# Kernel tuning notes

Measured on AMD Instinct MI355X. Metric: run time of the kernel, lower is better.

The kernel has to match this reference:

```python
import jax, jax.numpy as jnp
import numpy as np
import math

E = 8          # num_experts (= max_expert_num)
M = 1024       # hidden_size
H = 4096       # expert FFN dim (4*hidden)
B, S = 4, 4096 # batch, seq
CAP_FACTOR = 1.0
MIN_CAPACITY = 4


def setup_inputs() -> dict:
    key = jax.random.key(0)
    ks = jax.random.split(key, 5)
    hidden_states = jax.random.normal(ks[0], (B, S, M), dtype=jnp.float32)
    wg = jax.random.normal(ks[1], (M, E), dtype=jnp.float32) * (M ** -0.5)  # gate Linear (no bias, as in TopKGate)
    w1 = jax.random.normal(ks[2], (E, M, H), dtype=jnp.float32) * (M ** -0.5)
    b1 = jnp.zeros((E, H), dtype=jnp.float32)
    w2 = jax.random.normal(ks[3], (E, H, M), dtype=jnp.float32) * (H ** -0.5)
    b2 = jnp.zeros((E, M), dtype=jnp.float32)
    return {"hidden_states": hidden_states, "wg": wg, "w1": w1, "b1": b1, "w2": w2, "b2": b2}


def reference(hidden_states, wg, w1, b1, w2, b2):
    b, s_len, m = hidden_states.shape
    x = hidden_states.reshape(-1, m)            # [s, m], s = tokens
    s = x.shape[0]
    capacity = max(int(math.ceil(s / E * CAP_FACTOR)), MIN_CAPACITY)  # static

    # ---- top-1 gating (DeepSpeed top1gating, fp32, no jitter, no RTS) ----
    logits = x.astype(jnp.float32) @ wg          # [s, e]
    gates = jax.nn.softmax(logits, axis=1)
    idx = jnp.argmax(gates, axis=1)              # chosen expert per token
    mask1 = jax.nn.one_hot(idx, E, dtype=jnp.float32)
    exp_counts = jnp.sum(mask1, axis=0).astype(jnp.int32)
    ce = jnp.mean(mask1, axis=0)                 # fraction routed per expert (pre-drop)
    me = jnp.mean(gates, axis=0)
    l_aux = jnp.sum(me * ce) * E                 # load-balancing loss

    # position of each token within its expert's queue; drop past capacity
    locations = jnp.cumsum(mask1, axis=0) - 1.0  # [s, e]
    loc = jnp.sum(locations * mask1, axis=1).astype(jnp.int32)  # [s]
    keep = (loc < capacity).astype(jnp.float32)  # capacity drop mask
    gate_s = jnp.sum(gates * mask1, axis=1) * keep
    loc_c = jnp.clip(loc, 0, capacity - 1)

    # ---- dispatch: scatter tokens to [E, C, M] slots (equiv. to einsum('sec,sm->ecm')) ----
    dispatched = jnp.zeros((E, capacity, m), dtype=x.dtype).at[idx, loc_c].add(x * keep[:, None])

    # ---- grouped expert GEMMs (MLP with GELU) ----
    h = jax.nn.gelu(jnp.einsum('ecm,emh->ech', dispatched, w1) + b1[:, None, :])
    eout = jnp.einsum('ech,ehm->ecm', h, w2) + b2[:, None, :]

    # ---- combine: gather back and scale by gate value (dropped tokens -> 0) ----
    out = eout[idx, loc_c] * gate_s[:, None]     # [s, m]
    return out.reshape(b, s_len, m), l_aux, exp_counts
```

## Files before the change

### kernel.cpp

```cpp
#include <hip/hip_runtime.h>
#include <hip/hip_bf16.h>

#define TOKENS 16384
#define MDIM   1024
#define HDIM   4096
#define NEXP   8
#define EGRP   4
#define CAP    2048
#define NKT1   (MDIM / 64)
#define NKT2   (HDIM / 64)

typedef __attribute__((ext_vector_type(8))) short bf16x8;
typedef __attribute__((ext_vector_type(4))) float f32x4;

__device__ __forceinline__ short f2bf(float x) {
  unsigned u = __float_as_uint(x);
  unsigned r = (u + 0x7fffu + ((u >> 16) & 1u)) >> 16;
  return (short)r;
}

__device__ __forceinline__ unsigned bfbits(float x) {
  unsigned u = __float_as_uint(x);
  return u + 0x7fffu + ((u >> 16) & 1u);
}

__device__ __forceinline__ float gelu_f(float x) {
  float u = 1.5957691216057308f * (x + 0.044715f * x * x * x);
  float e = __expf(u);
  return x * (1.f - 1.f / (e + 1.f));
}

__global__ __launch_bounds__(256) void gating_kernel(
    const float* __restrict__ x, const float* __restrict__ wg,
    int* __restrict__ idx, float* __restrict__ gate,
    float* __restrict__ mepart, short* __restrict__ xb) {
  __shared__ float me_s[NEXP];
  int tid = threadIdx.x, wid = tid >> 6, lane = tid & 63;
  if (tid < NEXP) me_s[tid] = 0.f;
  __syncthreads();
  int t = blockIdx.x * 4 + wid;
  float acc[NEXP];
#pragma unroll
  for (int e = 0; e < NEXP; e++) acc[e] = 0.f;
  const float4* xr = (const float4*)(x + (size_t)t * MDIM);
  short* xbr = xb + (size_t)t * MDIM + lane * 16;
#pragma unroll
  for (int j = 0; j < 4; j++) {
    float4 xv = xr[lane * 4 + j];
    short4 bv; bv.x = f2bf(xv.x); bv.y = f2bf(xv.y); bv.z = f2bf(xv.z); bv.w = f2bf(xv.w);
    ((short4*)(xbr))[j] = bv;
    int base = lane * 16 + j * 4;
    const float* xp = &xv.x;
#pragma unroll
    for (int i = 0; i < 4; i++) {
      float xi = xp[i];
      const float4* wr = (const float4*)(wg + (size_t)(base + i) * NEXP);
      float4 w0 = wr[0], w1 = wr[1];
      acc[0] += xi * w0.x; acc[1] += xi * w0.y; acc[2] += xi * w0.z; acc[3] += xi * w0.w;
      acc[4] += xi * w1.x; acc[5] += xi * w1.y; acc[6] += xi * w1.z; acc[7] += xi * w1.w;
    }
  }
#pragma unroll
  for (int off = 32; off > 0; off >>= 1)
#pragma unroll
    for (int e = 0; e < NEXP; e++) acc[e] += __shfl_xor(acc[e], off, 64);
  if (lane == 0) {
    float mx = acc[0]; int ai = 0;
#pragma unroll
    for (int e = 1; e < NEXP; e++) if (acc[e] > mx) { mx = acc[e]; ai = e; }
    float ex[NEXP]; float se = 0.f;
#pragma unroll
    for (int e = 0; e < NEXP; e++) { ex[e] = __expf(acc[e] - mx); se += ex[e]; }
    float inv = 1.f / se;
#pragma unroll
    for (int e = 0; e < NEXP; e++) atomicAdd(&me_s[e], ex[e] * inv);
    idx[t] = ai;
    gate[t] = inv;
  }
  __syncthreads();
  if (tid < NEXP) mepart[blockIdx.x * NEXP + tid] = me_s[tid];
}

__global__ __launch_bounds__(1024) void scan_kernel(
    const int* __restrict__ idx, float* __restrict__ gate,
    int* __restrict__ s2t, int* __restrict__ counts) {
  __shared__ int wcnt[16][NEXP];
  __shared__ int wbase[16][NEXP];
  int tid = threadIdx.x, wid = tid >> 6, lane = tid & 63;
  unsigned long long ltmask = (1ull << lane) - 1ull;
  int myexp[16], myloc[16];
  int cnt[NEXP];
#pragma unroll
  for (int e = 0; e < NEXP; e++) cnt[e] = 0;
  int base_tok = wid * 1024;
#pragma unroll
  for (int p = 0; p < 16; p++) {
    int e = idx[base_tok + p * 64 + lane];
    myexp[p] = e;
    int pos = 0;
#pragma unroll
    for (int e2 = 0; e2 < NEXP; e2++) {
      unsigned long long b = __ballot(e == e2);
      if (e == e2) pos = cnt[e2] + __popcll(b & ltmask);
      cnt[e2] += __popcll(b);
    }
    myloc[p] = pos;
  }
  if (lane < NEXP) wcnt[wid][lane] = cnt[lane];
  __syncthreads();
  if (tid < 128) {
    int w = tid >> 3, e = tid & 7;
    int s = 0;
    for (int w2 = 0; w2 < w; w2++) s += wcnt[w2][e];
    wbase[w][e] = s;
  }
  __syncthreads();
#pragma unroll
  for (int p = 0; p < 16; p++) {
    int i = base_tok + p * 64 + lane;
    int e = myexp[p];
    int loc = wbase[wid][e] + myloc[p];
    if (loc < CAP) s2t[e * CAP + loc] = i;
    else           gate[i] = 0.f;
  }
  if (tid < NEXP) {
    int tot = 0;
#pragma unroll
    for (int w = 0; w < 16; w++) tot += wcnt[w][tid];
    counts[tid] = tot;
  }
}

__global__ __launch_bounds__(256) void finalize_kernel(
    const float* __restrict__ mepart, const int* __restrict__ counts,
    float* __restrict__ out_tail, int nblocks) {
  __shared__ float red[256];
  __shared__ float me[NEXP];
  int tid = threadIdx.x;
  float s = 0.f;
  int e = tid & 7;
  for (int r = tid >> 3; r < nblocks; r += 32) s += mepart[r * NEXP + e];
  red[tid] = s;
  __syncthreads();
  if (tid < NEXP) {
    float tsum = 0.f;
    for (int i = tid; i < 256; i += 8) tsum += red[i];
    me[tid] = tsum;
  }
  __syncthreads();
  if (tid == 0) {
    float la = 0.f;
    for (int k = 0; k < NEXP; k++)
      la += (me[k] / (float)TOKENS) * ((float)counts[k] / (float)TOKENS);
    out_tail[0] = la * (float)NEXP;
  }
  if (tid < NEXP) out_tail[1 + tid] = (float)counts[tid];
}

__global__ __launch_bounds__(256) void transpose_cvt_kernel(
    const float* __restrict__ in, short* __restrict__ out, int R, int Cc) {
  __shared__ short tile[64][72];
  int e = blockIdx.z;
  const float* in_e = in + (size_t)e * R * Cc;
  short* out_e = out + (size_t)e * R * Cc;
  int r0 = blockIdx.y * 64, c0 = blockIdx.x * 64;
  int tid = threadIdx.x;
#pragma unroll
  for (int i = 0; i < 4; i++) {
    int linear = tid + 256 * i;
    int r = linear >> 4;
    int f4 = linear & 15;
    float4 v = *(const float4*)(in_e + (size_t)(r0 + r) * Cc + c0 + f4 * 4);
    int c = f4 * 4;
    tile[c + 0][r] = f2bf(v.x);
    tile[c + 1][r] = f2bf(v.y);
    tile[c + 2][r] = f2bf(v.z);
    tile[c + 3][r] = f2bf(v.w);
  }
  __syncthreads();
#pragma unroll
  for (int i = 0; i < 4; i++) {
    int linear = tid + 256 * i;
    int c = linear >> 4;
    int s4 = linear & 15;
    short4 s;
    s.x = tile[c][s4 * 4 + 0]; s.y = tile[c][s4 * 4 + 1];
    s.z = tile[c][s4 * 4 + 2]; s.w = tile[c][s4 * 4 + 3];
    *(short4*)(out_e + (size_t)(c0 + c) * R + r0 + s4 * 4) = s;
  }
}

__device__ __forceinline__ void pe_vm8() {
  asm volatile("s_waitcnt vmcnt(8)" ::: "memory");
  __builtin_amdgcn_s_barrier();
  asm volatile("" ::: "memory");
}
__device__ __forceinline__ void pe_vm6() {
  asm volatile("s_waitcnt vmcnt(6)" ::: "memory");
  __builtin_amdgcn_s_barrier();
  asm volatile("" ::: "memory");
}
__device__ __forceinline__ void pe_vm0() {
  asm volatile("s_waitcnt vmcnt(0)" ::: "memory");
  __builtin_amdgcn_s_barrier();
  asm volatile("" ::: "memory");
}

#define GLL(gp, lp) __builtin_amdgcn_global_load_lds(                                   \
    (const __attribute__((address_space(1))) void*)(gp),                                \
    (__attribute__((address_space(3))) void*)(lp), 16, 0, 0)

__global__ __launch_bounds__(512, 2) void gemm1_kernel(
    const short* __restrict__ xb, const int* __restrict__ s2t,
    const short* __restrict__ W1t, const float* __restrict__ b1,
    short* __restrict__ Hh, const short* __restrict__ zrow, int eg) {
  __shared__ __align__(16) short ldsA[2][256 * 64];
  __shared__ __align__(16) short ldsB[2][256 * 64];
  int bz = blockIdx.z, bm = blockIdx.y, bn = blockIdx.x;
  int e_abs = eg + bz;
  int tid = threadIdx.x, lane = tid & 63, w = tid >> 6;
  int v = tid >> 3;
  int sl = tid & 7;

  const short* aptr[4];
#pragma unroll
  for (int q = 0; q < 4; q++) {
    int r = q * 64 + v;
    int tok = s2t[e_abs * CAP + bm * 256 + r];
    const short* basep = (tok >= 0) ? (xb + (size_t)tok * MDIM) : zrow;
    aptr[q] = basep + ((sl ^ (r & 7)) * 8);
  }
  const short* Be = W1t + ((size_t)e_abs * HDIM + (size_t)bn * 256) * MDIM;
  const short* bptr[2][2];
#pragma unroll
  for (int h = 0; h < 2; h++)
#pragma unroll
    for (int j = 0; j < 2; j++) {
      int r = j * 128 + (v >> 5) * 64 + (v & 31) + h * 32;
      bptr[h][j] = Be + (size_t)r * MDIM + ((sl ^ (r & 7)) * 8);
    }
  asm volatile("" ::: "memory");

  int ldsa_base[4], ldsb_base[2][2];
#pragma unroll
  for (int q = 0; q < 4; q++) ldsa_base[q] = (q * 64 + w * 8) * 64;
#pragma unroll
  for (int h = 0; h < 2; h++)
#pragma unroll
    for (int j = 0; j < 2; j++)
      ldsb_base[h][j] = (j * 128 + h * 32 + (w >> 2) * 64 + (w & 3) * 8) * 64;

  GLL(aptr[0] + 0,        &ldsA[0][ldsa_base[0]]);
  GLL(aptr[2] + 0,        &ldsA[0][ldsa_base[2]]);
  GLL(bptr[0][0] + 0,     &ldsB[0][ldsb_base[0][0]]);
  GLL(bptr[0][1] + 0,     &ldsB[0][ldsb_base[0][1]]);
  GLL(bptr[1][0] + 0,     &ldsB[0][ldsb_base[1][0]]);
  GLL(bptr[1][1] + 0,     &ldsB[0][ldsb_base[1][1]]);
  GLL(aptr[1] + 0,        &ldsA[0][ldsa_base[1]]);
  GLL(aptr[3] + 0,        &ldsA[0][ldsa_base[3]]);
  GLL(aptr[0] + 64,       &ldsA[1][ldsa_base[0]]);
  GLL(aptr[2] + 64,       &ldsA[1][ldsa_base[2]]);
  GLL(bptr[0][0] + 64,    &ldsB[1][ldsb_base[0][0]]);
  GLL(bptr[0][1] + 64,    &ldsB[1][ldsb_base[0][1]]);
  GLL(bptr[1][0] + 64,    &ldsB[1][ldsb_base[1][0]]);
  GLL(bptr[1][1] + 64,    &ldsB[1][ldsb_base[1][1]]);
  GLL(aptr[1] + 64,       &ldsA[1][ldsa_base[1]]);
  GLL(aptr[3] + 64,       &ldsA[1][ldsa_base[3]]);
  pe_vm8();

  int wm = w >> 2, wn = w & 3;
  int ln = lane & 15, q4 = lane >> 4;
  int offk0 = ((q4 ^ (lane & 7)) * 8);
  int offk1 = (((4 + q4) ^ (lane & 7)) * 8);
  int arowbase = wm * 128 + ln;
  int browbase = wn * 64 + ln;

  f32x4 acc[8][4];
  f32x4 zero = {0.f, 0.f, 0.f, 0.f};
#pragma unroll
  for (int a = 0; a < 8; a++)
#pragma unroll
    for (int b = 0; b < 4; b++) acc[a][b] = zero;

  for (int t = 0; t < NKT1; ++t) {
    int cur = t & 1;
    const short* La = ldsA[cur];
    const short* Lb = ldsB[cur];
    int kts = (t + 2) * 64;
    bool st = (t + 2) < NKT1;
    bool steady = t < (NKT1 - 2);
    bf16x8 af[4][2], bf0[2][2], bf1[2][2];
#pragma unroll
    for (int rt = 0; rt < 4; rt++) {
      int ro = (arowbase + rt * 16) * 64;
      af[rt][0] = *(const bf16x8*)(La + ro + offk0);
      af[rt][1] = *(const bf16x8*)(La + ro + offk1);
    }
#pragma unroll
    for (int c = 0; c < 2; c++) {
      int ro = (browbase + c * 16) * 64;
      bf0[c][0] = *(const bf16x8*)(Lb + ro + offk0);
      bf0[c][1] = *(const bf16x8*)(Lb + ro + offk1);
    }
    __builtin_amdgcn_s_setprio(1);
#pragma unroll
    for (int rt = 0; rt < 4; rt++)
#pragma unroll
      for (int c = 0; c < 2; c++) {
        acc[rt][c] = __builtin_amdgcn_mfma_f32_16x16x32_bf16(bf0[c][0], af[rt][0], acc[rt][c], 0, 0, 0);
        acc[rt][c] = __builtin_amdgcn_mfma_f32_16x16x32_bf16(bf0[c][1], af[rt][1], acc[rt][c], 0, 0, 0);
      }
    __builtin_amdgcn_s_setprio(0);
    if (steady) pe_vm8(); else pe_vm0();
#pragma unroll
    for (int c = 0; c < 2; c++) {
      int ro = (browbase + (c + 2) * 16) * 64;
      bf1[c][0] = *(const bf16x8*)(Lb + ro + offk0);
      bf1[c][1] = *(const bf16x8*)(Lb + ro + offk1);
    }
    if (st) {
      GLL(aptr[0] + kts,    &ldsA[cur][ldsa_base[0]]);
      GLL(aptr[2] + kts,    &ldsA[cur][ldsa_base[2]]);
      GLL(bptr[0][0] + kts, &ldsB[cur][ldsb_base[0][0]]);
      GLL(bptr[0][1] + kts, &ldsB[cur][ldsb_base[0][1]]);
    }
    __builtin_amdgcn_s_setprio(1);
#pragma unroll
    for (int rt = 0; rt < 4; rt++)
#pragma unroll
      for (int c = 0; c < 2; c++) {
        acc[rt][c + 2] = __builtin_amdgcn_mfma_f32_16x16x32_bf16(bf1[c][0], af[rt][0], acc[rt][c + 2], 0, 0, 0);
        acc[rt][c + 2] = __builtin_amdgcn_mfma_f32_16x16x32_bf16(bf1[c][1], af[rt][1], acc[rt][c + 2], 0, 0, 0);
      }
    __builtin_amdgcn_s_setprio(0);
    if (steady) pe_vm8(); else pe_vm0();
#pragma unroll
    for (int rt = 0; rt < 4; rt++) {
      int ro = (arowbase + 64 + rt * 16) * 64;
      af[rt][0] = *(const bf16x8*)(La + ro + offk0);
      af[rt][1] = *(const bf16x8*)(La + ro + offk1);
    }
    if (st) {
      GLL(bptr[1][0] + kts, &ldsB[cur][ldsb_base[1][0]]);
      GLL(bptr[1][1] + kts, &ldsB[cur][ldsb_base[1][1]]);
    }
    __builtin_amdgcn_s_setprio(1);
#pragma unroll
    for (int rt = 0; rt < 4; rt++)
#pragma unroll
      for (int c = 0; c < 2; c++) {
        acc[4 + rt][c] = __builtin_amdgcn_mfma_f32_16x16x32_bf16(bf0[c][0], af[rt][0], acc[4 + rt][c], 0, 0, 0);
        acc[4 + rt][c] = __builtin_amdgcn_mfma_f32_16x16x32_bf16(bf0[c][1], af[rt][1], acc[4 + rt][c], 0, 0, 0);
      }
    __builtin_amdgcn_s_setprio(0);
    if (steady) pe_vm8(); else pe_vm0();
    if (st) {
      GLL(aptr[1] + kts,    &ldsA[cur][ldsa_base[1]]);
      GLL(aptr[3] + kts,    &ldsA[cur][ldsa_base[3]]);
    }
    __builtin_amdgcn_s_setprio(1);
#pragma unroll
    for (int rt = 0; rt < 4; rt++)
#pragma unroll
      for (int c = 0; c < 2; c++) {
        acc[4 + rt][c + 2] = __builtin_amdgcn_mfma_f32_16x16x32_bf16(bf1[c][0], af[rt][0], acc[4 + rt][c + 2], 0, 0, 0);
        acc[4 + rt][c + 2] = __builtin_amdgcn_mfma_f32_16x16x32_bf16(bf1[c][1], af[rt][1], acc[4 + rt][c + 2], 0, 0, 0);
      }
    __builtin_amdgcn_s_setprio(0);
    if (steady) pe_vm8(); else pe_vm0();
  }

#pragma unroll
  for (int rt = 0; rt < 8; rt++) {
    int caprow = bm * 256 + wm * 128 + rt * 16 + ln;
    size_t rowoff = ((size_t)bz * CAP + caprow) * HDIM;
#pragma unroll
    for (int c = 0; c < 4; c++) {
      int colb = bn * 256 + wn * 64 + c * 16 + q4 * 4;
      float4 bias = *(const float4*)(b1 + (size_t)e_abs * HDIM + colb);
      unsigned u0 = bfbits(gelu_f(acc[rt][c][0] + bias.x));
      unsigned u1 = bfbits(gelu_f(acc[rt][c][1] + bias.y));
      unsigned u2 = bfbits(gelu_f(acc[rt][c][2] + bias.z));
      unsigned u3 = bfbits(gelu_f(acc[rt][c][3] + bias.w));
      uint2 pk;
      pk.x = __builtin_amdgcn_perm(u1, u0, 0x07060302u);
      pk.y = __builtin_amdgcn_perm(u3, u2, 0x07060302u);
      *(uint2*)(Hh + rowoff + colb) = pk;
    }
  }
}

__global__ __launch_bounds__(512, 2) void gemm2_kernel(
    const short* __restrict__ Hh, const short* __restrict__ W2t,
    const float* __restrict__ b2, const int* __restrict__ s2t,
    const float* __restrict__ gate, float* __restrict__ out, int eg) {
  __shared__ __align__(16) short ldsA[2][128 * 64];
  __shared__ __align__(16) short ldsB[2][256 * 64];
  int bz = blockIdx.z, bm = blockIdx.y, bn = blockIdx.x;
  int e_abs = eg + bz;
  int tid = threadIdx.x, lane = tid & 63, w = tid >> 6;
  int v = tid >> 3, sl = tid & 7;
  const short* Ae = Hh + ((size_t)bz * CAP + (size_t)bm * 128) * HDIM;
  const short* Be = W2t + ((size_t)e_abs * MDIM + (size_t)bn * 256) * HDIM;
  const short* aptr[2];
#pragma unroll
  for (int h = 0; h < 2; h++) {
    int r = (v >> 5) * 64 + (v & 31) + h * 32;
    aptr[h] = Ae + (size_t)r * HDIM + ((sl ^ (r & 7)) * 8);
  }
  const short* bptr[4];
#pragma unroll
  for (int q = 0; q < 4; q++) {
    int r = q * 64 + v;
    bptr[q] = Be + (size_t)r * HDIM + ((sl ^ (r & 7)) * 8);
  }
  int ldsa_base[2], ldsb_base[4];
#pragma unroll
  for (int h = 0; h < 2; h++) ldsa_base[h] = (h * 32 + (w >> 2) * 64 + (w & 3) * 8) * 64;
#pragma unroll
  for (int q = 0; q < 4; q++) ldsb_base[q] = (q * 64 + w * 8) * 64;

  GLL(aptr[0] + 0,  &ldsA[0][ldsa_base[0]]);
  GLL(bptr[0] + 0,  &ldsB[0][ldsb_base[0]]);
  GLL(bptr[1] + 0,  &ldsB[0][ldsb_base[1]]);
  GLL(bptr[2] + 0,  &ldsB[0][ldsb_base[2]]);
  GLL(bptr[3] + 0,  &ldsB[0][ldsb_base[3]]);
  GLL(aptr[1] + 0,  &ldsA[0][ldsa_base[1]]);
  GLL(aptr[0] + 64, &ldsA[1][ldsa_base[0]]);
  GLL(bptr[0] + 64, &ldsB[1][ldsb_base[0]]);
  GLL(bptr[1] + 64, &ldsB[1][ldsb_base[1]]);
  GLL(bptr[2] + 64, &ldsB[1][ldsb_base[2]]);
  GLL(bptr[3] + 64, &ldsB[1][ldsb_base[3]]);
  asm volatile("s_waitcnt vmcnt(5)" ::: "memory");
  __builtin_amdgcn_s_barrier();
  asm volatile("" ::: "memory");

  int wm = w >> 2, wn = w & 3;
  int ln = lane & 15, q4 = lane >> 4;
  int offk0 = ((q4 ^ (lane & 7)) * 8);
  int offk1 = (((4 + q4) ^ (lane & 7)) * 8);
  int arowbase = wm * 64 + ln;
  int browbase = wn * 64 + ln;

  f32x4 acc[4][4];
  f32x4 zero = {0.f, 0.f, 0.f, 0.f};
#pragma unroll
  for (int a = 0; a < 4; a++)
#pragma unroll
    for (int b = 0; b < 4; b++) acc[a][b] = zero;

  for (int t = 0; t < NKT2; ++t) {
    int cur = t & 1;
    const short* La = ldsA[cur];
    const short* Lb = ldsB[cur];
    bool steady = t < (NKT2 - 2);
    bf16x8 af[2][2], bf[4][2];
#pragma unroll
    for (int rt = 0; rt < 2; rt++) {
      int ro = (arowbase + rt * 16) * 64;
      af[rt][0] = *(const bf16x8*)(La + ro + offk0);
      af[rt][1] = *(const bf16x8*)(La + ro + offk1);
    }
#pragma unroll
    for (int c = 0; c < 4; c++) {
      int ro = (browbase + c * 16) * 64;
      bf[c][0] = *(const bf16x8*)(Lb + ro + offk0);
      bf[c][1] = *(const bf16x8*)(Lb + ro + offk1);
    }
    if (t + 1 < NKT2) { GLL(aptr[1] + (t + 1) * 64, &ldsA[cur ^ 1][ldsa_base[1]]); }
    __builtin_amdgcn_s_setprio(1);
#pragma unroll
    for (int rt = 0; rt < 2; rt++)
#pragma unroll
      for (int c = 0; c < 4; c++) {
        acc[rt][c] = __builtin_amdgcn_mfma_f32_16x16x32_bf16(bf[c][0], af[rt][0], acc[rt][c], 0, 0, 0);
        acc[rt][c] = __builtin_amdgcn_mfma_f32_16x16x32_bf16(bf[c][1], af[rt][1], acc[rt][c], 0, 0, 0);
      }
    __builtin_amdgcn_s_setprio(0);
    if (steady) pe_vm6(); else pe_vm0();
#pragma unroll
    for (int rt = 0; rt < 2; rt++) {
      int ro = (arowbase + 32 + rt * 16) * 64;
      af[rt][0] = *(const bf16x8*)(La + ro + offk0);
      af[rt][1] = *(const bf16x8*)(La + ro + offk1);
    }
    if (t + 2 < NKT2) {
      int kts = (t + 2) * 64;
      GLL(aptr[0] + kts, &ldsA[cur][ldsa_base[0]]);
      GLL(bptr[0] + kts, &ldsB[cur][ldsb_base[0]]);
      GLL(bptr[1] + kts, &ldsB[cur][ldsb_base[1]]);
      GLL(bptr[2] + kts, &ldsB[cur][ldsb_base[2]]);
      GLL(bptr[3] + kts, &ldsB[cur][ldsb_base[3]]);
    }
    __builtin_amdgcn_s_setprio(1);
#pragma unroll
    for (int rt = 0; rt < 2; rt++)
#pragma unroll
      for (int c = 0; c < 4; c++) {
        acc[2 + rt][c] = __builtin_amdgcn_mfma_f32_16x16x32_bf16(bf[c][0], af[rt][0], acc[2 + rt][c], 0, 0, 0);
        acc[2 + rt][c] = __builtin_amdgcn_mfma_f32_16x16x32_bf16(bf[c][1], af[rt][1], acc[2 + rt][c], 0, 0, 0);
      }
    __builtin_amdgcn_s_setprio(0);
    if (steady) pe_vm6(); else pe_vm0();
  }

#pragma unroll
  for (int rt = 0; rt < 4; rt++) {
    int caprow = bm * 128 + wm * 64 + rt * 16 + ln;
    int token = s2t[e_abs * CAP + caprow];
    if (token < 0) continue;
    float g = gate[token];
    float* orow = out + (size_t)token * MDIM;
#pragma unroll
    for (int c = 0; c < 4; c++) {
      int colb = bn * 256 + wn * 64 + c * 16 + q4 * 4;
      float4 bias = *(const float4*)(b2 + (size_t)e_abs * MDIM + colb);
      float4 vv;
      vv.x = (acc[rt][c][0] + bias.x) * g;
      vv.y = (acc[rt][c][1] + bias.y) * g;
      vv.z = (acc[rt][c][2] + bias.z) * g;
      vv.w = (acc[rt][c][3] + bias.w) * g;
      *(float4*)(orow + colb) = vv;
    }
  }
}

__global__ __launch_bounds__(256) void zerodrop_kernel(
    const float* __restrict__ gate, float* __restrict__ out) {
  int t = blockIdx.x;
  if (gate[t] != 0.f) return;
  float4 z = {0.f, 0.f, 0.f, 0.f};
  ((float4*)(out + (size_t)t * MDIM))[threadIdx.x] = z;
}

extern "C" void kernel_launch(void* const* d_in, const int* in_sizes, int n_in,
                              void* d_out, int out_size, void* d_ws, size_t ws_size,
                              hipStream_t stream) {
  const float* x  = (const float*)d_in[0];
  const float* wg = (const float*)d_in[1];
  const float* w1 = (const float*)d_in[2];
  const float* b1 = (const float*)d_in[3];
  const float* w2 = (const float*)d_in[4];
  const float* b2 = (const float*)d_in[5];
  float* out = (float*)d_out;

  char* ws = (char*)d_ws;
  size_t off = 0;
  auto alloc = [&](size_t n) { char* ptr = ws + off; off += (n + 255) & ~(size_t)255; return ptr; };
  short* W1t  = (short*)alloc((size_t)NEXP * MDIM * HDIM * 2);
  short* W2t  = (short*)alloc((size_t)NEXP * MDIM * HDIM * 2);
  short* Hh   = (short*)alloc((size_t)EGRP * CAP * HDIM * 2);
  short* xb   = (short*)alloc((size_t)TOKENS * MDIM * 2);
  short* zrow = (short*)alloc((size_t)MDIM * 2);
  int*   idx  = (int*)  alloc(TOKENS * 4);
  float* gate = (float*)alloc(TOKENS * 4);
  int*   s2t  = (int*)  alloc(NEXP * CAP * 4);
  float* mep  = (float*)alloc((TOKENS / 4) * NEXP * 4);
  int*   cnts = (int*)  alloc(NEXP * 4);
  if (ws_size < off) return;

  hipMemsetAsync(s2t, 0xFF, NEXP * CAP * 4, stream);
  hipMemsetAsync(zrow, 0, MDIM * 2, stream);

  gating_kernel<<<TOKENS / 4, 256, 0, stream>>>(x, wg, idx, gate, mep, xb);
  scan_kernel<<<1, 1024, 0, stream>>>(idx, gate, s2t, cnts);
  finalize_kernel<<<1, 256, 0, stream>>>(mep, cnts, out + (size_t)TOKENS * MDIM, TOKENS / 4);
  transpose_cvt_kernel<<<dim3(HDIM / 64, MDIM / 64, NEXP), 256, 0, stream>>>(w1, W1t, MDIM, HDIM);
  transpose_cvt_kernel<<<dim3(MDIM / 64, HDIM / 64, NEXP), 256, 0, stream>>>(w2, W2t, HDIM, MDIM);
  for (int g = 0; g < 2; g++) {
    gemm1_kernel<<<dim3(HDIM / 256, CAP / 256, EGRP), 512, 0, stream>>>(xb, s2t, W1t, b1, Hh, zrow, g * EGRP);
    gemm2_kernel<<<dim3(MDIM / 256, CAP / 128, EGRP), 512, 0, stream>>>(Hh, W2t, b2, s2t, gate, out, g * EGRP);
  }
  zerodrop_kernel<<<TOKENS, 256, 0, stream>>>(gate, out);
}
```

Measured before the change: 837.7 us.

## Restructure GEMM main loops into barrier-separated LDS-read/MFMA phases; fuse finalize into scan

Reorders the gemm1 and gemm2 inner loops so each MFMA cluster is preceded by a workgroup barrier and an explicit lgkmcnt(0) wait. Global-to-LDS prefetches are moved between the compute phases, and MFMAs are ordered k-outer. This aims at a ping-pong style schedule where LDS reads and issue of global loads don't interleave with MFMA bursts, at the cost of extra barriers per iteration. Separately, the l_aux/count finalize kernel is folded into the single-block scan kernel, removing one launch.

```diff
diff --git a/kernel.cpp b/kernel.cpp
--- a/kernel.cpp
+++ b/kernel.cpp
@@ -83,9 +83,12 @@
 
 __global__ __launch_bounds__(1024) void scan_kernel(
     const int* __restrict__ idx, float* __restrict__ gate,
-    int* __restrict__ s2t, int* __restrict__ counts) {
+    int* __restrict__ s2t, int* __restrict__ counts,
+    const float* __restrict__ mepart, float* __restrict__ out_tail) {
   __shared__ int wcnt[16][NEXP];
   __shared__ int wbase[16][NEXP];
+  __shared__ int totc[NEXP];
+  __shared__ float red2[1024];
   int tid = threadIdx.x, wid = tid >> 6, lane = tid & 63;
   unsigned long long ltmask = (1ull << lane) - 1ull;
   int myexp[16], myloc[16];
@@ -128,33 +131,25 @@
 #pragma unroll
     for (int w = 0; w < 16; w++) tot += wcnt[w][tid];
     counts[tid] = tot;
-  }
-}
-
-__global__ __launch_bounds__(256) void finalize_kernel(
-    const float* __restrict__ mepart, const int* __restrict__ counts,
-    float* __restrict__ out_tail, int nblocks) {
-  __shared__ float red[256];
-  __shared__ float me[NEXP];
-  int tid = threadIdx.x;
+    totc[tid] = tot;
+  }
   float s = 0.f;
-  int e = tid & 7;
-  for (int r = tid >> 3; r < nblocks; r += 32) s += mepart[r * NEXP + e];
-  red[tid] = s;
+  int e2 = tid & 7;
+  for (int r = tid >> 3; r < (TOKENS / 4); r += 128) s += mepart[(size_t)r * NEXP + e2];
+  red2[tid] = s;
   __syncthreads();
-  if (tid < NEXP) {
-    float tsum = 0.f;
-    for (int i = tid; i < 256; i += 8) tsum += red[i];
-    me[tid] = tsum;
-  }
-  __syncthreads();
+#pragma unroll
+  for (int off = 512; off >= 8; off >>= 1) {
+    if (tid < off) red2[tid] += red2[tid + off];
+    __syncthreads();
+  }
   if (tid == 0) {
     float la = 0.f;
     for (int k = 0; k < NEXP; k++)
-      la += (me[k] / (float)TOKENS) * ((float)counts[k] / (float)TOKENS);
+      la += (red2[k] / (float)TOKENS) * ((float)totc[k] / (float)TOKENS);
     out_tail[0] = la * (float)NEXP;
   }
-  if (tid < NEXP) out_tail[1 + tid] = (float)counts[tid];
+  if (tid < NEXP) out_tail[1 + tid] = (float)totc[tid];
 }
 
 __global__ __launch_bounds__(256) void transpose_cvt_kernel(
@@ -190,17 +185,26 @@
   }
 }
 
-__device__ __forceinline__ void pe_vm8() {
+__device__ __forceinline__ void bar() {
+  asm volatile("" ::: "memory");
+  __builtin_amdgcn_s_barrier();
+  asm volatile("" ::: "memory");
+}
+__device__ __forceinline__ void lgkm0() {
+  asm volatile("s_waitcnt lgkmcnt(0)" ::: "memory");
+  __builtin_amdgcn_sched_barrier(0);
+}
+__device__ __forceinline__ void vm_bar8() {
   asm volatile("s_waitcnt vmcnt(8)" ::: "memory");
   __builtin_amdgcn_s_barrier();
   asm volatile("" ::: "memory");
 }
-__device__ __forceinline__ void pe_vm6() {
+__device__ __forceinline__ void vm_bar6() {
   asm volatile("s_waitcnt vmcnt(6)" ::: "memory");
   __builtin_amdgcn_s_barrier();
   asm volatile("" ::: "memory");
 }
-__device__ __forceinline__ void pe_vm0() {
+__device__ __forceinline__ void vm_bar0() {
   asm volatile("s_waitcnt vmcnt(0)" ::: "memory");
   __builtin_amdgcn_s_barrier();
   asm volatile("" ::: "memory");
@@ -266,7 +270,7 @@
   GLL(bptr[1][1] + 64,    &ldsB[1][ldsb_base[1][1]]);
   GLL(aptr[1] + 64,       &ldsA[1][ldsa_base[1]]);
   GLL(aptr[3] + 64,       &ldsA[1][ldsa_base[3]]);
-  pe_vm8();
+  vm_bar8();
 
   int wm = w >> 2, wn = w & 3;
   int ln = lane & 15, q4 = lane >> 4;
@@ -302,72 +306,80 @@
       bf0[c][0] = *(const bf16x8*)(Lb + ro + offk0);
       bf0[c][1] = *(const bf16x8*)(Lb + ro + offk1);
     }
+    bar();
+    lgkm0();
     __builtin_amdgcn_s_setprio(1);
 #pragma unroll
-    for (int rt = 0; rt < 4; rt++)
-#pragma unroll
-      for (int c = 0; c < 2; c++) {
-        acc[rt][c] = __builtin_amdgcn_mfma_f32_16x16x32_bf16(bf0[c][0], af[rt][0], acc[rt][c], 0, 0, 0);
-        acc[rt][c] = __builtin_amdgcn_mfma_f32_16x16x32_bf16(bf0[c][1], af[rt][1], acc[rt][c], 0, 0, 0);
-      }
+    for (int kk = 0; kk < 2; kk++)
+#pragma unroll
+      for (int rt = 0; rt < 4; rt++)
+#pragma unroll
+        for (int c = 0; c < 2; c++)
+          acc[rt][c] = __builtin_amdgcn_mfma_f32_16x16x32_bf16(bf0[c][kk], af[rt][kk], acc[rt][c], 0, 0, 0);
     __builtin_amdgcn_s_setprio(0);
-    if (steady) pe_vm8(); else pe_vm0();
-#pragma unroll
-    for (int c = 0; c < 2; c++) {
-      int ro = (browbase + (c + 2) * 16) * 64;
-      bf1[c][0] = *(const bf16x8*)(Lb + ro + offk0);
-      bf1[c][1] = *(const bf16x8*)(Lb + ro + offk1);
-    }
+    bar();
     if (st) {
       GLL(aptr[0] + kts,    &ldsA[cur][ldsa_base[0]]);
       GLL(aptr[2] + kts,    &ldsA[cur][ldsa_base[2]]);
       GLL(bptr[0][0] + kts, &ldsB[cur][ldsb_base[0][0]]);
       GLL(bptr[0][1] + kts, &ldsB[cur][ldsb_base[0][1]]);
     }
+#pragma unroll
+    for (int c = 0; c < 2; c++) {
+      int ro = (browbase + (c + 2) * 16) * 64;
+      bf1[c][0] = *(const bf16x8*)(Lb + ro + offk0);
+      bf1[c][1] = *(const bf16x8*)(Lb + ro + offk1);
+    }
+    bar();
+    lgkm0();
     __builtin_amdgcn_s_setprio(1);
 #pragma unroll
-    for (int rt = 0; rt < 4; rt++)
-#pragma unroll
-      for (int c = 0; c < 2; c++) {
-        acc[rt][c + 2] = __builtin_amdgcn_mfma_f32_16x16x32_bf16(bf1[c][0], af[rt][0], acc[rt][c + 2], 0, 0, 0);
-        acc[rt][c + 2] = __builtin_amdgcn_mfma_f32_16x16x32_bf16(bf1[c][1], af[rt][1], acc[rt][c + 2], 0, 0, 0);
-      }
+    for (int kk = 0; kk < 2; kk++)
+#pragma unroll
+      for (int rt = 0; rt < 4; rt++)
+#pragma unroll
+        for (int c = 0; c < 2; c++)
+          acc[rt][c + 2] = __builtin_amdgcn_mfma_f32_16x16x32_bf16(bf1[c][kk], af[rt][kk], acc[rt][c + 2], 0, 0, 0);
     __builtin_amdgcn_s_setprio(0);
-    if (steady) pe_vm8(); else pe_vm0();
+    bar();
+    if (st) {
+      GLL(bptr[1][0] + kts, &ldsB[cur][ldsb_base[1][0]]);
+      GLL(bptr[1][1] + kts, &ldsB[cur][ldsb_base[1][1]]);
+    }
 #pragma unroll
     for (int rt = 0; rt < 4; rt++) {
       int ro = (arowbase + 64 + rt * 16) * 64;
       af[rt][0] = *(const bf16x8*)(La + ro + offk0);
       af[rt][1] = *(const bf16x8*)(La + ro + offk1);
     }
-    if (st) {
-      GLL(bptr[1][0] + kts, &ldsB[cur][ldsb_base[1][0]]);
-      GLL(bptr[1][1] + kts, &ldsB[cur][ldsb_base[1][1]]);
-    }
+    bar();
+    lgkm0();
     __builtin_amdgcn_s_setprio(1);
 #pragma unroll
-    for (int rt = 0; rt < 4; rt++)
-#pragma unroll
-      for (int c = 0; c < 2; c++) {
-        acc[4 + rt][c] = __builtin_amdgcn_mfma_f32_16x16x32_bf16(bf0[c][0], af[rt][0], acc[4 + rt][c], 0, 0, 0);
-        acc[4 + rt][c] = __builtin_amdgcn_mfma_f32_16x16x32_bf16(bf0[c][1], af[rt][1], acc[4 + rt][c], 0, 0, 0);
-      }
+    for (int kk = 0; kk < 2; kk++)
+#pragma unroll
+      for (int rt = 0; rt < 4; rt++)
+#pragma unroll
+        for (int c = 0; c < 2; c++)
+          acc[4 + rt][c] = __builtin_amdgcn_mfma_f32_16x16x32_bf16(bf0[c][kk], af[rt][kk], acc[4 + rt][c], 0, 0, 0);
     __builtin_amdgcn_s_setprio(0);
-    if (steady) pe_vm8(); else pe_vm0();
+    bar();
     if (st) {
       GLL(aptr[1] + kts,    &ldsA[cur][ldsa_base[1]]);
       GLL(aptr[3] + kts,    &ldsA[cur][ldsa_base[3]]);
     }
+    bar();
+    lgkm0();
     __builtin_amdgcn_s_setprio(1);
 #pragma unroll
-    for (int rt = 0; rt < 4; rt++)
-#pragma unroll
-      for (int c = 0; c < 2; c++) {
-        acc[4 + rt][c + 2] = __builtin_amdgcn_mfma_f32_16x16x32_bf16(bf1[c][0], af[rt][0], acc[4 + rt][c + 2], 0, 0, 0);
-        acc[4 + rt][c + 2] = __builtin_amdgcn_mfma_f32_16x16x32_bf16(bf1[c][1], af[rt][1], acc[4 + rt][c + 2], 0, 0, 0);
-      }
+    for (int kk = 0; kk < 2; kk++)
+#pragma unroll
+      for (int rt = 0; rt < 4; rt++)
+#pragma unroll
+        for (int c = 0; c < 2; c++)
+          acc[4 + rt][c + 2] = __builtin_amdgcn_mfma_f32_16x16x32_bf16(bf1[c][kk], af[rt][kk], acc[4 + rt][c + 2], 0, 0, 0);
     __builtin_amdgcn_s_setprio(0);
-    if (steady) pe_vm8(); else pe_vm0();
+    if (steady) vm_bar8(); else vm_bar0();
   }
 
 #pragma unroll
@@ -455,6 +467,7 @@
     const short* Lb = ldsB[cur];
     bool steady = t < (NKT2 - 2);
     bf16x8 af[2][2], bf[4][2];
+    if (t + 1 < NKT2) { GLL(aptr[1] + (t + 1) * 64, &ldsA[cur ^ 1][ldsa_base[1]]); }
 #pragma unroll
     for (int rt = 0; rt < 2; rt++) {
       int ro = (arowbase + rt * 16) * 64;
@@ -467,23 +480,18 @@
       bf[c][0] = *(const bf16x8*)(Lb + ro + offk0);
       bf[c][1] = *(const bf16x8*)(Lb + ro + offk1);
     }
-    if (t + 1 < NKT2) { GLL(aptr[1] + (t + 1) * 64, &ldsA[cur ^ 1][ldsa_base[1]]); }
+    bar();
+    lgkm0();
     __builtin_amdgcn_s_setprio(1);
 #pragma unroll
-    for (int rt = 0; rt < 2; rt++)
-#pragma unroll
-      for (int c = 0; c < 4; c++) {
-        acc[rt][c] = __builtin_amdgcn_mfma_f32_16x16x32_bf16(bf[c][0], af[rt][0], acc[rt][c], 0, 0, 0);
-        acc[rt][c] = __builtin_amdgcn_mfma_f32_16x16x32_bf16(bf[c][1], af[rt][1], acc[rt][c], 0, 0, 0);
-      }
+    for (int kk = 0; kk < 2; kk++)
+#pragma unroll
+      for (int rt = 0; rt < 2; rt++)
+#pragma unroll
+        for (int c = 0; c < 4; c++)
+          acc[rt][c] = __builtin_amdgcn_mfma_f32_16x16x32_bf16(bf[c][kk], af[rt][kk], acc[rt][c], 0, 0, 0);
     __builtin_amdgcn_s_setprio(0);
-    if (steady) pe_vm6(); else pe_vm0();
-#pragma unroll
-    for (int rt = 0; rt < 2; rt++) {
-      int ro = (arowbase + 32 + rt * 16) * 64;
-      af[rt][0] = *(const bf16x8*)(La + ro + offk0);
-      af[rt][1] = *(const bf16x8*)(La + ro + offk1);
-    }
+    if (steady) vm_bar6(); else vm_bar0();
     if (t + 2 < NKT2) {
       int kts = (t + 2) * 64;
       GLL(aptr[0] + kts, &ldsA[cur][ldsa_base[0]]);
@@ -492,16 +500,24 @@
       GLL(bptr[2] + kts, &ldsB[cur][ldsb_base[2]]);
       GLL(bptr[3] + kts, &ldsB[cur][ldsb_base[3]]);
     }
+#pragma unroll
+    for (int rt = 0; rt < 2; rt++) {
+      int ro = (arowbase + 32 + rt * 16) * 64;
+      af[rt][0] = *(const bf16x8*)(La + ro + offk0);
+      af[rt][1] = *(const bf16x8*)(La + ro + offk1);
+    }
+    bar();
+    lgkm0();
     __builtin_amdgcn_s_setprio(1);
 #pragma unroll
-    for (int rt = 0; rt < 2; rt++)
-#pragma unroll
-      for (int c = 0; c < 4; c++) {
-        acc[2 + rt][c] = __builtin_amdgcn_mfma_f32_16x16x32_bf16(bf[c][0], af[rt][0], acc[2 + rt][c], 0, 0, 0);
-        acc[2 + rt][c] = __builtin_amdgcn_mfma_f32_16x16x32_bf16(bf[c][1], af[rt][1], acc[2 + rt][c], 0, 0, 0);
-      }
+    for (int kk = 0; kk < 2; kk++)
+#pragma unroll
+      for (int rt = 0; rt < 2; rt++)
+#pragma unroll
+        for (int c = 0; c < 4; c++)
+          acc[2 + rt][c] = __builtin_amdgcn_mfma_f32_16x16x32_bf16(bf[c][kk], af[rt][kk], acc[2 + rt][c], 0, 0, 0);
     __builtin_amdgcn_s_setprio(0);
-    if (steady) pe_vm6(); else pe_vm0();
+    if (steady) vm_bar6(); else vm_bar0();
   }
 
 #pragma unroll
@@ -563,8 +579,7 @@
   hipMemsetAsync(zrow, 0, MDIM * 2, stream);
 
   gating_kernel<<<TOKENS / 4, 256, 0, stream>>>(x, wg, idx, gate, mep, xb);
-  scan_kernel<<<1, 1024, 0, stream>>>(idx, gate, s2t, cnts);
-  finalize_kernel<<<1, 256, 0, stream>>>(mep, cnts, out + (size_t)TOKENS * MDIM, TOKENS / 4);
+  scan_kernel<<<1, 1024, 0, stream>>>(idx, gate, s2t, cnts, mep, out + (size_t)TOKENS * MDIM);
   transpose_cvt_kernel<<<dim3(HDIM / 64, MDIM / 64, NEXP), 256, 0, stream>>>(w1, W1t, MDIM, HDIM);
   transpose_cvt_kernel<<<dim3(MDIM / 64, HDIM / 64, NEXP), 256, 0, stream>>>(w2, W2t, HDIM, MDIM);
   for (int g = 0; g < 2; g++) {
```

After: 933.3 us. 11.4% more time.
